# Optimization experiments

Measured on AMD Instinct MI355X. Metric: run time of the kernel, lower is better.

## Reference

```python
import jax, jax.numpy as jnp
import numpy as np

D_MODEL = 512
N_HEADS = 4
D_HEAD = D_MODEL // N_HEADS
D_FF = 2048
N_LAYERS = 3
IN_DIM = 25
OUT_DIM = 1
PRE = 20          # pre_training_size
SCALE = 10.0      # scaling_factor
EPS = 1e-5


def setup_inputs() -> dict:
    key = jax.random.key(0)
    ks = jax.random.split(key, 20)
    B, S = 4, 2048
    def gn(k, shape, fan_in):
        return jax.random.normal(k, shape, jnp.float32) * (1.0 / np.sqrt(fan_in))
    return {
        "src": jax.random.normal(ks[0], (B, S, IN_DIM), jnp.float32),
        "emb_w": gn(ks[1], (D_MODEL, IN_DIM), IN_DIM),
        "emb_b": jnp.zeros((D_MODEL,), jnp.float32),
        "in_w": gn(ks[2], (N_LAYERS, 3 * D_MODEL, D_MODEL), D_MODEL),
        "in_b": jnp.zeros((N_LAYERS, 3 * D_MODEL), jnp.float32),
        "out_w": gn(ks[3], (N_LAYERS, D_MODEL, D_MODEL), D_MODEL),
        "out_b": jnp.zeros((N_LAYERS, D_MODEL), jnp.float32),
        "ln1_g": jnp.ones((N_LAYERS, D_MODEL), jnp.float32),
        "ln1_b": jnp.zeros((N_LAYERS, D_MODEL), jnp.float32),
        "ln2_g": jnp.ones((N_LAYERS, D_MODEL), jnp.float32),
        "ln2_b": jnp.zeros((N_LAYERS, D_MODEL), jnp.float32),
        "ff1_w": gn(ks[4], (N_LAYERS, D_FF, D_MODEL), D_MODEL),
        "ff1_b": jnp.zeros((N_LAYERS, D_FF), jnp.float32),
        "ff2_w": gn(ks[5], (N_LAYERS, D_MODEL, D_FF), D_FF),
        "ff2_b": jnp.zeros((N_LAYERS, D_MODEL), jnp.float32),
        "dec_w": gn(ks[6], (OUT_DIM, D_MODEL), D_MODEL),
        "dec_b": jnp.zeros((OUT_DIM,), jnp.float32),
    }


def _layer_norm(x, g, b):
    mu = jnp.mean(x, axis=-1, keepdims=True)
    var = jnp.var(x, axis=-1, keepdims=True)
    return (x - mu) * jax.lax.rsqrt(var + EPS) * g + b


def _pos_encoding(seq_len):
    # eval mode: start index 0, no dropout
    pos = jnp.arange(seq_len, dtype=jnp.float32)[:, None]           # [S,1]
    div = jnp.exp(jnp.arange(0, D_MODEL, 2, dtype=jnp.float32) * (-np.log(10000.0) / D_MODEL))  # [D/2]
    ang = pos * div                                                  # [S,D/2]
    return jnp.stack([jnp.sin(ang), jnp.cos(ang)], axis=-1).reshape(seq_len, D_MODEL)


def _causal_mask(seq_len):
    row = jnp.arange(seq_len)[:, None]
    col = jnp.arange(seq_len)[None, :]
    mask = jnp.where(col <= row, 0.0, -jnp.inf).astype(jnp.float32)
    # include_training_period=True: first PRE x PRE block unmasked
    return mask.at[:PRE, :PRE].set(0.0)


def reference(src, emb_w, emb_b, in_w, in_b, out_w, out_b,
              ln1_g, ln1_b, ln2_g, ln2_b, ff1_w, ff1_b, ff2_w, ff2_b,
              dec_w, dec_b):
    B, S, _ = src.shape
    x = src @ emb_w.T + emb_b                    # [B,S,D]
    x = x + _pos_encoding(S)[None]
    mask = _causal_mask(S)                       # [S,S]
    scale = 1.0 / np.sqrt(D_HEAD)
    for l in range(N_LAYERS):
        # --- self-attention (post-norm, eager bmm+softmax+bmm path) ---
        qkv = x @ in_w[l].T + in_b[l]            # [B,S,3D]
        q, k, v = jnp.split(qkv, 3, axis=-1)
        q = q.reshape(B, S, N_HEADS, D_HEAD).transpose(0, 2, 1, 3)
        k = k.reshape(B, S, N_HEADS, D_HEAD).transpose(0, 2, 1, 3)
        v = v.reshape(B, S, N_HEADS, D_HEAD).transpose(0, 2, 1, 3)
        scores = jnp.einsum('bhqd,bhkd->bhqk', q, k) * scale + mask
        attn = jax.nn.softmax(scores, axis=-1)   # [B,H,S,S] (need_weights=True path)
        o = jnp.einsum('bhqk,bhkd->bhqd', attn, v)
        o = o.transpose(0, 2, 1, 3).reshape(B, S, D_MODEL)
        o = o @ out_w[l].T + out_b[l]
        x = _layer_norm(x + o, ln1_g[l], ln1_b[l])
        # --- FFN ---
        h = jax.nn.relu(x @ ff1_w[l].T + ff1_b[l])
        h = h @ ff2_w[l].T + ff2_b[l]
        x = _layer_norm(x + h, ln2_g[l], ln2_b[l])
    out = jnp.tanh(x @ dec_w.T + dec_b) * SCALE  # [B,S,1]
    return out
```

## Files before the change

### kernel.cpp

```cpp
#include <hip/hip_runtime.h>

#define S_LEN 2048
#define DMODEL 512

typedef __attribute__((ext_vector_type(8))) short bf16x8;
typedef __attribute__((ext_vector_type(4))) float f32x4;
typedef __attribute__((ext_vector_type(4))) unsigned short u16x4;
typedef __attribute__((ext_vector_type(8))) unsigned short u16x8;
typedef __attribute__((ext_vector_type(2))) unsigned int u32x2;

__device__ __forceinline__ unsigned short f2bf(float f) {
    unsigned int u = __float_as_uint(f);
    u += 0x7fff + ((u >> 16) & 1);
    return (unsigned short)(u >> 16);
}
__device__ __forceinline__ float bf2f(unsigned short h) {
    return __uint_as_float(((unsigned int)h) << 16);
}
__device__ __forceinline__ void gll16(const void* g, void* l) {
    __builtin_amdgcn_global_load_lds(
        (const __attribute__((address_space(1))) unsigned int*)g,
        (__attribute__((address_space(3))) unsigned int*)l, 16, 0, 0);
}

__global__ __launch_bounds__(256) void conv_all(
    const float4* __restrict__ in_w, const float4* __restrict__ out_w,
    const float4* __restrict__ ff1_w, const float4* __restrict__ ff2_w,
    u16x4* __restrict__ in_wb, u16x4* __restrict__ out_wb,
    u16x4* __restrict__ ff1_wb, u16x4* __restrict__ ff2_wb)
{
    int i = blockIdx.x * 256 + threadIdx.x;
    const float4* src; u16x4* dst; int j;
    if (i < 589824)        { src = in_w;  dst = in_wb;  j = i; }
    else if (i < 786432)   { src = out_w; dst = out_wb; j = i - 589824; }
    else if (i < 1572864)  { src = ff1_w; dst = ff1_wb; j = i - 786432; }
    else                   { src = ff2_w; dst = ff2_wb; j = i - 1572864; }
    float4 v = src[j];
    u16x4 o = { f2bf(v.x), f2bf(v.y), f2bf(v.z), f2bf(v.w) };
    dst[j] = o;
}

__global__ __launch_bounds__(256) void embed_kernel(
    const float* __restrict__ src, const float* __restrict__ ew,
    const float* __restrict__ eb, float* __restrict__ X,
    unsigned short* __restrict__ Xb)
{
    int rid = blockIdx.x;
    int s = rid & (S_LEN - 1);
    int tid = threadIdx.x;
    __shared__ float sr[25];
    if (tid < 25) sr[tid] = src[rid * 25 + tid];
    __syncthreads();
    #pragma unroll
    for (int rep = 0; rep < 2; rep++) {
        int d = tid + rep * 256;
        float a = eb[d];
        #pragma unroll
        for (int k = 0; k < 25; k++) a = fmaf(sr[k], ew[d * 25 + k], a);
        int i2 = d & ~1;
        float div = expf(-(float)i2 * (9.210340371976184f / 512.f));
        float ang = (float)s * div;
        a += (d & 1) ? cosf(ang) : sinf(ang);
        X[(size_t)rid * DMODEL + d] = a;
        Xb[(size_t)rid * DMODEL + d] = f2bf(a);
    }
}

template<int MODE, int BN>
__global__ __launch_bounds__(256) void gemm_bf16(
    const unsigned short* __restrict__ A, int lda,
    const unsigned short* __restrict__ W, int K,
    const float* __restrict__ bias,
    unsigned short* __restrict__ out, int ldc,
    unsigned short* __restrict__ out2)
{
    constexpr int NJ = BN / 32;
    __shared__ __align__(16) unsigned short As[2][128 * 64];
    __shared__ __align__(16) unsigned short Ws[2][BN * 64];
    int tid = threadIdx.x;
    int lane = tid & 63, w = tid >> 6;
    int g = lane >> 4, c15 = lane & 15;
    int wm = w >> 1, wn = w & 1;
    int bm, bn;
    if (BN == 64) {
        int raw = blockIdx.x;
        int lid = ((raw & 7) << 6) | (raw >> 3);
        bn = lid & 7; bm = lid >> 3;
    } else {
        bm = blockIdx.y; bn = blockIdx.x;
    }

    f32x4 acc[4][NJ];
    #pragma unroll
    for (int i = 0; i < 4; i++)
        #pragma unroll
        for (int j = 0; j < NJ; j++) acc[i][j] = (f32x4){0.f, 0.f, 0.f, 0.f};

    auto stage = [&](int kk, int bi) {
        #pragma unroll
        for (int i = 0; i < 4; i++) {
            int chunk = tid + i * 256;
            int r = chunk >> 3, c = chunk & 7;
            int cs = c ^ (r & 7);
            gll16(A + (size_t)(bm * 128 + r) * lda + kk * 64 + cs * 8,
                  (void*)(As[bi] + chunk * 8));
        }
        #pragma unroll
        for (int i = 0; i < BN / 32; i++) {
            int chunk = tid + i * 256;
            int r = chunk >> 3, c = chunk & 7;
            int cs = c ^ (r & 7);
            gll16(W + (size_t)(bn * BN + r) * K + kk * 64 + cs * 8,
                  (void*)(Ws[bi] + chunk * 8));
        }
    };

    const int nk = K >> 6;
    stage(0, 0);
    __syncthreads();
    int buf = 0;

    for (int kk = 0; kk < nk; kk++) {
        if (kk + 1 < nk) stage(kk + 1, buf ^ 1);
        bf16x8 a[4][2], b[NJ][2];
        #pragma unroll
        for (int mi = 0; mi < 4; mi++) {
            int row = wm * 64 + mi * 16 + c15;
            #pragma unroll
            for (int h = 0; h < 2; h++) {
                int ck = (h * 4 + g) ^ (row & 7);
                a[mi][h] = *(const bf16x8*)((const char*)As[buf] + row * 128 + ck * 16);
            }
        }
        #pragma unroll
        for (int nj = 0; nj < NJ; nj++) {
            int row = wn * (BN / 2) + nj * 16 + c15;
            #pragma unroll
            for (int h = 0; h < 2; h++) {
                int ck = (h * 4 + g) ^ (row & 7);
                b[nj][h] = *(const bf16x8*)((const char*)Ws[buf] + row * 128 + ck * 16);
            }
        }
        __builtin_amdgcn_s_setprio(1);
        #pragma unroll
        for (int h = 0; h < 2; h++)
            #pragma unroll
            for (int mi = 0; mi < 4; mi++)
                #pragma unroll
                for (int nj = 0; nj < NJ; nj++)
                    acc[mi][nj] = __builtin_amdgcn_mfma_f32_16x16x32_bf16(
                        a[mi][h], b[nj][h], acc[mi][nj], 0, 0, 0);
        __builtin_amdgcn_s_setprio(0);
        __syncthreads();
        buf ^= 1;
    }
    #pragma unroll
    for (int nj = 0; nj < NJ; nj++) {
        int colb = bn * BN + wn * (BN / 2) + nj * 16;
        float bv = bias[colb + c15];
        #pragma unroll
        for (int mi = 0; mi < 4; mi++) {
            int rowb = bm * 128 + wm * 64 + mi * 16 + g * 4;
            if (MODE == 3 && colb >= 1024) {
                int cv = colb - 1024 + c15;
                int hh = cv >> 7, d = cv & 127;
                int bb = rowb >> 11, t = rowb & (S_LEN - 1);
                u16x4 pk;
                #pragma unroll
                for (int r = 0; r < 4; r++) pk[r] = f2bf(acc[mi][nj][r] + bv);
                *(u16x4*)(out2 + ((size_t)(bb * 4 + hh) * 128 + d) * S_LEN + t) = pk;
            } else {
                #pragma unroll
                for (int r = 0; r < 4; r++) {
                    float v = acc[mi][nj][r] + bv;
                    if (MODE == 2) v = fmaxf(v, 0.f);
                    out[(size_t)(rowb + r) * ldc + colb + c15] = f2bf(v);
                }
            }
        }
    }
}

__global__ __launch_bounds__(256) void flash_attn(
    const unsigned short* __restrict__ QKb,
    const unsigned short* __restrict__ Vt,
    unsigned short* __restrict__ Ob,
    unsigned short* __restrict__ Opart,
    float* __restrict__ Mpart,
    float* __restrict__ Lpart)
{
    __shared__ __align__(16) unsigned short Ks[2][32 * 128];
    __shared__ __align__(16) unsigned short Vts[2][128 * 32];
    __shared__ __align__(16) unsigned short Plds[4][16 * 40];
    const float scale = 0.08838834764831845f;
    int tid = threadIdx.x;
    int lane = tid & 63, w = tid >> 6;
    int g = lane >> 4, c15 = lane & 15;
    int raw = blockIdx.x;
    int lid = (raw & 7) * 96 + (raw >> 3);
    int bh = lid / 48, idx = lid - bh * 48;
    int b = bh >> 2, h = bh & 3;
    int qb, kt0, nkt, split;
    if (idx < 16) { qb = idx; kt0 = 0; nkt = 2 * qb + 2; split = -1; }
    else {
        int s = idx - 16;
        qb = 16 + (s >> 1);
        int j = s & 1;
        kt0 = j * (qb + 1);
        nkt = qb + 1;
        split = bh * 32 + (qb - 16) * 2 + j;
    }

    bf16x8 q[4];
    {
        const unsigned short* qrow =
            QKb + (size_t)(b * S_LEN + qb * 64 + w * 16 + c15) * 1024 + h * 128;
        #pragma unroll
        for (int k0 = 0; k0 < 4; k0++) q[k0] = *(const bf16x8*)(qrow + k0 * 32 + g * 8);
    }
    f32x4 o[8];
    #pragma unroll
    for (int cd = 0; cd < 8; cd++) o[cd] = (f32x4){0.f, 0.f, 0.f, 0.f};
    float m = -3e38f, l = 0.f;

    auto stage = [&](int kt, int bi) {
        #pragma unroll
        for (int i = 0; i < 2; i++) {
            int chunk = tid + i * 256;
            int r = chunk >> 4, c = chunk & 15;
            int cs = (c & 8) | ((c ^ r) & 7);
            gll16(QKb + (size_t)(b * S_LEN + kt * 32 + r) * 1024 + 512 + h * 128 + cs * 8,
                  (void*)(Ks[bi] + chunk * 8));
        }
        #pragma unroll
        for (int i = 0; i < 2; i++) {
            int chunk = tid + i * 256;
            int r = chunk >> 2, c = chunk & 3;
            int cs = (c ^ r) & 3;
            gll16(Vt + ((size_t)(b * 4 + h) * 128 + r) * S_LEN + kt * 32 + cs * 8,
                  (void*)(Vts[bi] + chunk * 8));
        }
    };

    stage(kt0, 0);
    __syncthreads();
    int buf = 0;

    for (int t = 0; t < nkt; t++) {
        int kt = kt0 + t;
        if (t + 1 < nkt) stage(kt + 1, buf ^ 1);
        f32x4 sf[2];
        __builtin_amdgcn_s_setprio(1);
        #pragma unroll
        for (int c = 0; c < 2; c++) {
            sf[c] = (f32x4){0.f, 0.f, 0.f, 0.f};
            int tok16 = c * 16 + c15;
            #pragma unroll
            for (int k0 = 0; k0 < 4; k0++) {
                int ck = k0 * 4 + g;
                int cs = (ck & 8) | ((ck ^ tok16) & 7);
                bf16x8 kf = *(const bf16x8*)((const char*)Ks[buf] + tok16 * 256 + cs * 16);
                sf[c] = __builtin_amdgcn_mfma_f32_16x16x32_bf16(kf, q[k0], sf[c], 0, 0, 0);
            }
        }
        __builtin_amdgcn_s_setprio(0);
        if (kt >= 2 * qb) {
            int qr = qb * 64 + w * 16 + c15;
            #pragma unroll
            for (int c = 0; c < 2; c++)
                #pragma unroll
                for (int r = 0; r < 4; r++) {
                    int tok = kt * 32 + c * 16 + g * 4 + r;
                    bool ok = (tok <= qr) || (qr < 20 && tok < 20);
                    if (!ok) sf[c][r] = -3e38f;
                }
        }
        float t0 = fmaxf(fmaxf(sf[0][0], sf[0][1]), fmaxf(sf[0][2], sf[0][3]));
        float t1 = fmaxf(fmaxf(sf[1][0], sf[1][1]), fmaxf(sf[1][2], sf[1][3]));
        float mt = fmaxf(t0, t1);
        mt = fmaxf(mt, __shfl_xor(mt, 16));
        mt = fmaxf(mt, __shfl_xor(mt, 32));
        bool need = !__all(mt <= m + 90.5f);
        float sc = 1.f;
        if (need) {
            float mn = fmaxf(m, mt);
            sc = __expf((m - mn) * scale);
            m = mn;
        }
        float msc = m * scale;
        #pragma unroll
        for (int c = 0; c < 2; c++)
            #pragma unroll
            for (int r = 0; r < 4; r++)
                sf[c][r] = __expf(fmaf(sf[c][r], scale, -msc));
        float s0 = (sf[0][0] + sf[0][1]) + (sf[0][2] + sf[0][3]);
        float s1 = (sf[1][0] + sf[1][1]) + (sf[1][2] + sf[1][3]);
        float ls = s0 + s1;
        ls += __shfl_xor(ls, 16);
        ls += __shfl_xor(ls, 32);
        if (need) l *= sc;
        l += ls;
        #pragma unroll
        for (int c = 0; c < 2; c++) {
            unsigned int lo = ((unsigned int)f2bf(sf[c][1]) << 16) | f2bf(sf[c][0]);
            unsigned int hi = ((unsigned int)f2bf(sf[c][3]) << 16) | f2bf(sf[c][2]);
            u32x2 pk = {lo, hi};
            *(u32x2*)&Plds[w][c15 * 40 + c * 16 + g * 4] = pk;
        }
        if (need) {
            float r0 = __shfl(sc, g * 4 + 0);
            float r1 = __shfl(sc, g * 4 + 1);
            float r2 = __shfl(sc, g * 4 + 2);
            float r3 = __shfl(sc, g * 4 + 3);
            #pragma unroll
            for (int cd = 0; cd < 8; cd++) {
                o[cd][0] *= r0; o[cd][1] *= r1; o[cd][2] *= r2; o[cd][3] *= r3;
            }
        }
        bf16x8 pa = *(const bf16x8*)((const char*)&Plds[w][0] + c15 * 80 + g * 16);
        __builtin_amdgcn_s_setprio(1);
        #pragma unroll
        for (int cd = 0; cd < 8; cd++) {
            int dv = cd * 16 + c15;
            int cs = (g ^ dv) & 3;
            bf16x8 vf = *(const bf16x8*)((const char*)Vts[buf] + dv * 64 + cs * 16);
            o[cd] = __builtin_amdgcn_mfma_f32_16x16x32_bf16(pa, vf, o[cd], 0, 0, 0);
        }
        __builtin_amdgcn_s_setprio(0);
        __syncthreads();
        buf ^= 1;
    }

    if (split < 0) {
        float li0 = 1.f / __shfl(l, g * 4 + 0);
        float li1 = 1.f / __shfl(l, g * 4 + 1);
        float li2 = 1.f / __shfl(l, g * 4 + 2);
        float li3 = 1.f / __shfl(l, g * 4 + 3);
        size_t obase = (size_t)(b * S_LEN + qb * 64 + w * 16 + g * 4) * 512 + h * 128;
        #pragma unroll
        for (int cd = 0; cd < 8; cd++) {
            Ob[obase + 0 * 512 + cd * 16 + c15] = f2bf(o[cd][0] * li0);
            Ob[obase + 1 * 512 + cd * 16 + c15] = f2bf(o[cd][1] * li1);
            Ob[obase + 2 * 512 + cd * 16 + c15] = f2bf(o[cd][2] * li2);
            Ob[obase + 3 * 512 + cd * 16 + c15] = f2bf(o[cd][3] * li3);
        }
    } else {
        unsigned short* op = Opart + (size_t)split * 8192;
        int rb = w * 16 + g * 4;
        #pragma unroll
        for (int cd = 0; cd < 8; cd++) {
            op[(rb + 0) * 128 + cd * 16 + c15] = f2bf(o[cd][0]);
            op[(rb + 1) * 128 + cd * 16 + c15] = f2bf(o[cd][1]);
            op[(rb + 2) * 128 + cd * 16 + c15] = f2bf(o[cd][2]);
            op[(rb + 3) * 128 + cd * 16 + c15] = f2bf(o[cd][3]);
        }
        if (g == 0) {
            Mpart[split * 64 + w * 16 + c15] = m;
            Lpart[split * 64 + w * 16 + c15] = l;
        }
    }
}

__global__ __launch_bounds__(256) void attn_merge(
    const unsigned short* __restrict__ Opart,
    const float* __restrict__ Mpart, const float* __restrict__ Lpart,
    unsigned short* __restrict__ Ob)
{
    const float scale = 0.08838834764831845f;
    int bid = blockIdx.x;
    int bh = bid >> 4, qe = bid & 15;
    int qb = 16 + qe;
    int b = bh >> 2, h = bh & 3;
    int p0 = bh * 32 + qe * 2;
    int t = threadIdx.x;
    int r = t >> 2, dq = t & 3;
    float m0 = Mpart[p0 * 64 + r], m1 = Mpart[(p0 + 1) * 64 + r];
    float l0 = Lpart[p0 * 64 + r], l1 = Lpart[(p0 + 1) * 64 + r];
    float ms = fmaxf(m0, m1);
    float w0 = __expf((m0 - ms) * scale), w1 = __expf((m1 - ms) * scale);
    float linv = 1.f / (l0 * w0 + l1 * w1);
    w0 *= linv; w1 *= linv;
    const unsigned short* o0 = Opart + (size_t)p0 * 8192 + r * 128 + dq * 32;
    const unsigned short* o1 = o0 + 8192;
    unsigned short* od = Ob + (size_t)(b * S_LEN + qb * 64 + r) * 512 + h * 128 + dq * 32;
    #pragma unroll
    for (int i = 0; i < 4; i++) {
        u16x8 a = *(const u16x8*)(o0 + i * 8);
        u16x8 c = *(const u16x8*)(o1 + i * 8);
        u16x8 d;
        #pragma unroll
        for (int j = 0; j < 8; j++)
            d[j] = f2bf(bf2f(a[j]) * w0 + bf2f(c[j]) * w1);
        *(u16x8*)(od + i * 8) = d;
    }
}

__global__ __launch_bounds__(256) void add_ln_kernel(
    float* __restrict__ X, const unsigned short* __restrict__ D,
    const float* __restrict__ gw, const float* __restrict__ bw,
    unsigned short* __restrict__ Xb)
{
    int row = blockIdx.x;
    int tid = threadIdx.x;
    size_t base = (size_t)row * DMODEL;
    float v0 = X[base + tid] + bf2f(D[base + tid]);
    float v1 = X[base + tid + 256] + bf2f(D[base + tid + 256]);
    float s = v0 + v1;
    float sq = v0 * v0 + v1 * v1;
    #pragma unroll
    for (int off = 32; off > 0; off >>= 1) {
        s  += __shfl_down(s, off);
        sq += __shfl_down(sq, off);
    }
    __shared__ float red[2][4];
    int wv = tid >> 6;
    if ((tid & 63) == 0) { red[0][wv] = s; red[1][wv] = sq; }
    __syncthreads();
    s  = red[0][0] + red[0][1] + red[0][2] + red[0][3];
    sq = red[1][0] + red[1][1] + red[1][2] + red[1][3];
    float mu = s * (1.f / DMODEL);
    float var = sq * (1.f / DMODEL) - mu * mu;
    float rs = rsqrtf(var + 1e-5f);
    float y0 = (v0 - mu) * rs * gw[tid] + bw[tid];
    float y1 = (v1 - mu) * rs * gw[tid + 256] + bw[tid + 256];
    X[base + tid] = y0;
    X[base + tid + 256] = y1;
    Xb[base + tid] = f2bf(y0);
    Xb[base + tid + 256] = f2bf(y1);
}

__global__ __launch_bounds__(256) void decoder_kernel(
    const float* __restrict__ X, const float* __restrict__ w,
    const float* __restrict__ bias, float* __restrict__ out)
{
    int tid = threadIdx.x;
    int lane = tid & 63;
    int row = blockIdx.x * 4 + (tid >> 6);
    float s = 0.f;
    size_t base = (size_t)row * DMODEL;
    #pragma unroll
    for (int i = 0; i < 8; i++) s = fmaf(X[base + lane + i * 64], w[lane + i * 64], s);
    #pragma unroll
    for (int off = 32; off > 0; off >>= 1) s += __shfl_down(s, off);
    if (lane == 0) out[row] = tanhf(s + bias[0]) * 10.0f;
}

extern "C" void kernel_launch(void* const* d_in, const int* in_sizes, int n_in,
                              void* d_out, int out_size, void* d_ws, size_t ws_size,
                              hipStream_t stream)
{
    const float* src   = (const float*)d_in[0];
    const float* emb_w = (const float*)d_in[1];
    const float* emb_b = (const float*)d_in[2];
    const float* in_w  = (const float*)d_in[3];
    const float* in_b  = (const float*)d_in[4];
    const float* out_w = (const float*)d_in[5];
    const float* out_b = (const float*)d_in[6];
    const float* ln1_g = (const float*)d_in[7];
    const float* ln1_b = (const float*)d_in[8];
    const float* ln2_g = (const float*)d_in[9];
    const float* ln2_b = (const float*)d_in[10];
    const float* ff1_w = (const float*)d_in[11];
    const float* ff1_b = (const float*)d_in[12];
    const float* ff2_w = (const float*)d_in[13];
    const float* ff2_b = (const float*)d_in[14];
    const float* dec_w = (const float*)d_in[15];
    const float* dec_b = (const float*)d_in[16];

    char* ws = (char*)d_ws;
    float*          X   = (float*)ws;
    unsigned short* Xb  = (unsigned short*)(ws + (16u << 20));
    unsigned short* Pb  = (unsigned short*)(ws + (24u << 20));
    unsigned short* Ob  = (unsigned short*)(ws + (32u << 20));
    unsigned short* QKb = (unsigned short*)(ws + (40u << 20));
    unsigned short* Vt  = (unsigned short*)(ws + (56u << 20));
    unsigned short* Hb  = (unsigned short*)(ws + (40u << 20));
    unsigned short* Opart = (unsigned short*)(ws + (16u << 20));
    float* Mpart = (float*)(ws + (24u << 20));
    float* Lpart = Mpart + 512 * 64;
    unsigned short* in_wb  = (unsigned short*)(ws + (72u << 20));
    unsigned short* out_wb = in_wb  + 3u * 1536 * 512;
    unsigned short* ff1_wb = out_wb + 3u * 512 * 512;
    unsigned short* ff2_wb = ff1_wb + 3u * 2048 * 512;
    float* outp = (float*)d_out;
    const int M = 4 * S_LEN;

    conv_all<<<9216, 256, 0, stream>>>(
        (const float4*)in_w, (const float4*)out_w,
        (const float4*)ff1_w, (const float4*)ff2_w,
        (u16x4*)in_wb, (u16x4*)out_wb, (u16x4*)ff1_wb, (u16x4*)ff2_wb);

    embed_kernel<<<M, 256, 0, stream>>>(src, emb_w, emb_b, X, Xb);

    for (int l = 0; l < 3; l++) {
        gemm_bf16<3, 128><<<dim3(12, 64), 256, 0, stream>>>(
            Xb, 512, in_wb + (size_t)l * 1536 * 512, 512, in_b + l * 1536,
            QKb, 1024, Vt);
        flash_attn<<<768, 256, 0, stream>>>(QKb, Vt, Ob, Opart, Mpart, Lpart);
        attn_merge<<<256, 256, 0, stream>>>(Opart, Mpart, Lpart, Ob);
        gemm_bf16<1, 64><<<dim3(512), 256, 0, stream>>>(
            Ob, 512, out_wb + (size_t)l * 512 * 512, 512, out_b + l * 512,
            Pb, 512, nullptr);
        add_ln_kernel<<<M, 256, 0, stream>>>(X, Pb, ln1_g + l * 512, ln1_b + l * 512, Xb);
        gemm_bf16<2, 128><<<dim3(16, 64), 256, 0, stream>>>(
            Xb, 512, ff1_wb + (size_t)l * 2048 * 512, 512, ff1_b + l * 2048,
            Hb, 2048, nullptr);
        gemm_bf16<1, 64><<<dim3(512), 256, 0, stream>>>(
            Hb, 2048, ff2_wb + (size_t)l * 512 * 2048, 2048, ff2_b + l * 512,
            Pb, 512, nullptr);
        add_ln_kernel<<<M, 256, 0, stream>>>(X, Pb, ln2_g + l * 512, ln2_b + l * 512, Xb);
    }

    decoder_kernel<<<M / 4, 256, 0, stream>>>(X, dec_w, dec_b, outp);
}
```

Before: 547.1 us.

## Rebalance flash-attention split-K into up to four chunks and fold softmax scale into Q

Flash attention now splits query blocks into 1 to 4 key-range chunks according to causal length, so each work item covers a similar span of keys. This grows the grid from 768 to 1088 blocks, and the merge kernel now combines up to four partials. The softmax scale times log2(e) is folded into Q inside the QKV GEMM epilogue, so the inner loop uses a bare exp2 with no per-element multiply. P is packed to bf16 with a hardware pack instruction. The trade-offs are more partial-output traffic, a heavier merge step, and Q stored in bf16 after scaling, which slightly changes rounding.

New measurement: 554.7 us. Within noise of the previous version (+1.4%).

```diff
diff --git a/kernel.cpp b/kernel.cpp
--- a/kernel.cpp
+++ b/kernel.cpp
@@ -2,6 +2,7 @@
 
 #define S_LEN 2048
 #define DMODEL 512
+#define QS 0.12751742795f
 
 typedef __attribute__((ext_vector_type(8))) short bf16x8;
 typedef __attribute__((ext_vector_type(4))) float f32x4;
@@ -16,6 +17,11 @@
 }
 __device__ __forceinline__ float bf2f(unsigned short h) {
     return __uint_as_float(((unsigned int)h) << 16);
+}
+__device__ __forceinline__ unsigned int cvtpk(float lo, float hi) {
+    unsigned int r;
+    asm("v_cvt_pk_bf16_f32 %0, %1, %2" : "=v"(r) : "v"(lo), "v"(hi));
+    return r;
 }
 __device__ __forceinline__ void gll16(const void* g, void* l) {
     __builtin_amdgcn_global_load_lds(
@@ -174,6 +180,7 @@
                 for (int r = 0; r < 4; r++) {
                     float v = acc[mi][nj][r] + bv;
                     if (MODE == 2) v = fmaxf(v, 0.f);
+                    if (MODE == 3 && colb < 512) v *= QS;
                     out[(size_t)(rowb + r) * ldc + colb + c15] = f2bf(v);
                 }
             }
@@ -192,23 +199,26 @@
     __shared__ __align__(16) unsigned short Ks[2][32 * 128];
     __shared__ __align__(16) unsigned short Vts[2][128 * 32];
     __shared__ __align__(16) unsigned short Plds[4][16 * 40];
-    const float scale = 0.08838834764831845f;
     int tid = threadIdx.x;
     int lane = tid & 63, w = tid >> 6;
     int g = lane >> 4, c15 = lane & 15;
     int raw = blockIdx.x;
-    int lid = (raw & 7) * 96 + (raw >> 3);
-    int bh = lid / 48, idx = lid - bh * 48;
+    int lid = (raw & 7) * 136 + (raw >> 3);
+    int bh = lid / 68, idx = lid - bh * 68;
     int b = bh >> 2, h = bh & 3;
-    int qb, kt0, nkt, split;
-    if (idx < 16) { qb = idx; kt0 = 0; nkt = 2 * qb + 2; split = -1; }
+    int qb, j, nc;
+    if (idx < 10)      { qb = idx; j = 0; nc = 1; }
+    else if (idx < 30) { int s = idx - 10; qb = 10 + (s >> 1); j = s & 1; nc = 2; }
+    else if (idx < 60) { int s = idx - 30; qb = 20 + s / 3;    j = s - (qb - 20) * 3; nc = 3; }
+    else               { int s = idx - 60; qb = 30 + (s >> 2); j = s & 3; nc = 4; }
+    int T = 2 * qb + 2;
+    int kt0 = j * T / nc;
+    int nkt = (j + 1) * T / nc - kt0;
+    int split;
+    if (nc == 1) split = -1;
     else {
-        int s = idx - 16;
-        qb = 16 + (s >> 1);
-        int j = s & 1;
-        kt0 = j * (qb + 1);
-        nkt = qb + 1;
-        split = bh * 32 + (qb - 16) * 2 + j;
+        int off = (qb < 20) ? 2 * (qb - 10) : (qb < 30 ? 20 + 3 * (qb - 20) : 50 + 4 * (qb - 30));
+        split = bh * 58 + off + j;
     }
 
     bf16x8 q[4];
@@ -280,19 +290,18 @@
         float mt = fmaxf(t0, t1);
         mt = fmaxf(mt, __shfl_xor(mt, 16));
         mt = fmaxf(mt, __shfl_xor(mt, 32));
-        bool need = !__all(mt <= m + 90.5f);
+        bool need = !__all(mt <= m + 11.5f);
         float sc = 1.f;
         if (need) {
             float mn = fmaxf(m, mt);
-            sc = __expf((m - mn) * scale);
+            sc = __builtin_amdgcn_exp2f(m - mn);
             m = mn;
         }
-        float msc = m * scale;
         #pragma unroll
         for (int c = 0; c < 2; c++)
             #pragma unroll
             for (int r = 0; r < 4; r++)
-                sf[c][r] = __expf(fmaf(sf[c][r], scale, -msc));
+                sf[c][r] = __builtin_amdgcn_exp2f(sf[c][r] - m);
         float s0 = (sf[0][0] + sf[0][1]) + (sf[0][2] + sf[0][3]);
         float s1 = (sf[1][0] + sf[1][1]) + (sf[1][2] + sf[1][3]);
         float ls = s0 + s1;
@@ -302,9 +311,7 @@
         l += ls;
         #pragma unroll
         for (int c = 0; c < 2; c++) {
-            unsigned int lo = ((unsigned int)f2bf(sf[c][1]) << 16) | f2bf(sf[c][0]);
-            unsigned int hi = ((unsigned int)f2bf(sf[c][3]) << 16) | f2bf(sf[c][2]);
-            u32x2 pk = {lo, hi};
+            u32x2 pk = { cvtpk(sf[c][0], sf[c][1]), cvtpk(sf[c][2], sf[c][3]) };
             *(u32x2*)&Plds[w][c15 * 40 + c * 16 + g * 4] = pk;
         }
         if (need) {
@@ -366,31 +373,49 @@
     const float* __restrict__ Mpart, const float* __restrict__ Lpart,
     unsigned short* __restrict__ Ob)
 {
-    const float scale = 0.08838834764831845f;
     int bid = blockIdx.x;
-    int bh = bid >> 4, qe = bid & 15;
-    int qb = 16 + qe;
+    int bh = bid / 22, qe = bid - bh * 22;
+    int qb = 10 + qe;
     int b = bh >> 2, h = bh & 3;
-    int p0 = bh * 32 + qe * 2;
+    int nc = (qb < 20) ? 2 : (qb < 30 ? 3 : 4);
+    int off = (qb < 20) ? 2 * (qb - 10) : (qb < 30 ? 20 + 3 * (qb - 20) : 50 + 4 * (qb - 30));
+    int p0 = bh * 58 + off;
     int t = threadIdx.x;
     int r = t >> 2, dq = t & 3;
-    float m0 = Mpart[p0 * 64 + r], m1 = Mpart[(p0 + 1) * 64 + r];
-    float l0 = Lpart[p0 * 64 + r], l1 = Lpart[(p0 + 1) * 64 + r];
-    float ms = fmaxf(m0, m1);
-    float w0 = __expf((m0 - ms) * scale), w1 = __expf((m1 - ms) * scale);
-    float linv = 1.f / (l0 * w0 + l1 * w1);
-    w0 *= linv; w1 *= linv;
-    const unsigned short* o0 = Opart + (size_t)p0 * 8192 + r * 128 + dq * 32;
-    const unsigned short* o1 = o0 + 8192;
+    float mi[4], li[4], wi[4];
+    #pragma unroll
+    for (int i = 0; i < 4; i++) {
+        mi[i] = (i < nc) ? Mpart[(p0 + i) * 64 + r] : -3e38f;
+        li[i] = (i < nc) ? Lpart[(p0 + i) * 64 + r] : 0.f;
+    }
+    float ms = fmaxf(fmaxf(mi[0], mi[1]), fmaxf(mi[2], mi[3]));
+    float lsum = 0.f;
+    #pragma unroll
+    for (int i = 0; i < 4; i++) {
+        wi[i] = (i < nc) ? __builtin_amdgcn_exp2f(mi[i] - ms) : 0.f;
+        lsum += li[i] * wi[i];
+    }
+    float linv = 1.f / lsum;
+    #pragma unroll
+    for (int i = 0; i < 4; i++) wi[i] *= linv;
     unsigned short* od = Ob + (size_t)(b * S_LEN + qb * 64 + r) * 512 + h * 128 + dq * 32;
+    size_t obase = (size_t)p0 * 8192 + r * 128 + dq * 32;
     #pragma unroll
     for (int i = 0; i < 4; i++) {
-        u16x8 a = *(const u16x8*)(o0 + i * 8);
-        u16x8 c = *(const u16x8*)(o1 + i * 8);
         u16x8 d;
-        #pragma unroll
-        for (int j = 0; j < 8; j++)
-            d[j] = f2bf(bf2f(a[j]) * w0 + bf2f(c[j]) * w1);
+        float acc[8];
+        #pragma unroll
+        for (int jj = 0; jj < 8; jj++) acc[jj] = 0.f;
+        #pragma unroll
+        for (int p = 0; p < 4; p++) {
+            if (p < nc) {
+                u16x8 a = *(const u16x8*)(Opart + obase + (size_t)p * 8192 + i * 8);
+                #pragma unroll
+                for (int jj = 0; jj < 8; jj++) acc[jj] += bf2f(a[jj]) * wi[p];
+            }
+        }
+        #pragma unroll
+        for (int jj = 0; jj < 8; jj++) d[jj] = f2bf(acc[jj]);
         *(u16x8*)(od + i * 8) = d;
     }
 }
@@ -476,8 +501,8 @@
     unsigned short* Vt  = (unsigned short*)(ws + (56u << 20));
     unsigned short* Hb  = (unsigned short*)(ws + (40u << 20));
     unsigned short* Opart = (unsigned short*)(ws + (16u << 20));
-    float* Mpart = (float*)(ws + (24u << 20));
-    float* Lpart = Mpart + 512 * 64;
+    float* Mpart = (float*)(ws + (31u << 20));
+    float* Lpart = Mpart + 928 * 64;
     unsigned short* in_wb  = (unsigned short*)(ws + (72u << 20));
     unsigned short* out_wb = in_wb  + 3u * 1536 * 512;
     unsigned short* ff1_wb = out_wb + 3u * 512 * 512;
@@ -496,8 +521,8 @@
         gemm_bf16<3, 128><<<dim3(12, 64), 256, 0, stream>>>(
             Xb, 512, in_wb + (size_t)l * 1536 * 512, 512, in_b + l * 1536,
             QKb, 1024, Vt);
-        flash_attn<<<768, 256, 0, stream>>>(QKb, Vt, Ob, Opart, Mpart, Lpart);
-        attn_merge<<<256, 256, 0, stream>>>(Opart, Mpart, Lpart, Ob);
+        flash_attn<<<1088, 256, 0, stream>>>(QKb, Vt, Ob, Opart, Mpart, Lpart);
+        attn_merge<<<352, 256, 0, stream>>>(Opart, Mpart, Lpart, Ob);
         gemm_bf16<1, 64><<<dim3(512), 256, 0, stream>>>(
             Ob, 512, out_wb + (size_t)l * 512 * 512, 512, out_b + l * 512,
             Pb, 512, nullptr);
```
